# Performance work log

Measured on AMD Instinct MI355X. Metric: run time of the kernel, lower is better.

## Reference

```python
import jax, jax.numpy as jnp
import numpy as np

WS = 8          # cubic window side
HEADS = 6
DIM = 192


def _make_buffers(ws=WS):
    # relative_coords_table: [1, 2w-1, 2w-1, 2w-1, 3], signed log-spaced in [-1,1]*? (Swin V2)
    c = np.arange(-(ws - 1), ws, dtype=np.float32)
    g = np.stack(np.meshgrid(c, c, c, indexing='ij'), axis=-1)[None]  # [1,15,15,15,3]
    g = g / (ws - 1) * 8.0
    table = np.sign(g) * np.log2(np.abs(g) + 1.0) / np.log2(8.0)
    # relative_position_index: [N, N] into the (2w-1)^3 table
    coords = np.stack(np.meshgrid(np.arange(ws), np.arange(ws), np.arange(ws), indexing='ij'))
    cf = coords.reshape(3, -1)                          # [3, N]
    rel = cf[:, :, None] - cf[:, None, :]               # [3, N, N]
    rel = rel.transpose(1, 2, 0) + (ws - 1)             # [N, N, 3]
    idx = rel[..., 0] * (2 * ws - 1) ** 2 + rel[..., 1] * (2 * ws - 1) + rel[..., 2]
    return table.astype(np.float32), idx.astype(np.int32)


def setup_inputs() -> dict:
    key = jax.random.key(0)
    ks = jax.random.split(key, 8)
    B_, N, C, nW = 64, WS ** 3, DIM, 16
    table, idx = _make_buffers()
    return {
        'x': jax.random.normal(ks[0], (B_, N, C), jnp.float32),
        'mask': jax.random.normal(ks[1], (nW, N, N), jnp.float32),
        'qkv_w': jax.random.normal(ks[2], (3 * C, C), jnp.float32) * 0.05,
        'q_bias': jnp.zeros((C,), jnp.float32),
        'v_bias': jnp.zeros((C,), jnp.float32),
        'logit_scale': jnp.log(10.0) * jnp.ones((HEADS, 1, 1), jnp.float32),
        'cpb_w1': jax.random.normal(ks[3], (512, 3), jnp.float32) * 0.1,
        'cpb_b1': jnp.zeros((512,), jnp.float32),
        'cpb_w2': jax.random.normal(ks[4], (HEADS, 512), jnp.float32) * 0.1,
        'proj_w': jax.random.normal(ks[5], (C, C), jnp.float32) * 0.05,
        'proj_b': jnp.zeros((C,), jnp.float32),
        'rel_table': jnp.asarray(table),
        'rel_index': jnp.asarray(idx),
    }


def reference(x, mask, qkv_w, q_bias, v_bias, logit_scale, cpb_w1, cpb_b1,
              cpb_w2, proj_w, proj_b, rel_table, rel_index):
    B_, N, C = x.shape
    H = HEADS
    hd = C // H
    # qkv projection with (q_bias, 0, v_bias)
    qkv_b = jnp.concatenate([q_bias, jnp.zeros_like(v_bias), v_bias])
    qkv = (x @ qkv_w.T + qkv_b).reshape(B_, N, 3, H, hd).transpose(2, 0, 3, 1, 4)
    q, k, v = qkv[0], qkv[1], qkv[2]                 # each [B_, H, N, hd]
    # cosine attention with clamped learned logit scale
    qn = q / jnp.maximum(jnp.linalg.norm(q, axis=-1, keepdims=True), 1e-12)
    kn = k / jnp.maximum(jnp.linalg.norm(k, axis=-1, keepdims=True), 1e-12)
    scale = jnp.exp(jnp.minimum(logit_scale, jnp.log(100.0)))  # [H,1,1]
    attn = jnp.einsum('bhnd,bhmd->bhnm', qn, kn) * scale[None]
    # continuous position bias: MLP over coords table, gather by relative index
    hidden = jax.nn.relu(rel_table @ cpb_w1.T + cpb_b1)        # [1,15,15,15,512]
    tbl = (hidden @ cpb_w2.T).reshape(-1, H)                   # [3375, H]
    bias = tbl[rel_index.reshape(-1)].reshape(N, N, H).transpose(2, 0, 1)
    bias = 16.0 * jax.nn.sigmoid(bias)                         # [H, N, N]
    attn = attn + bias[None]
    # window mask
    nW = mask.shape[0]
    attn = attn.reshape(B_ // nW, nW, H, N, N) + mask[None, :, None]
    attn = jax.nn.softmax(attn.reshape(B_, H, N, N), axis=-1)
    out = jnp.einsum('bhnm,bhmd->bhnd', attn, v)
    out = out.transpose(0, 2, 1, 3).reshape(B_, N, C)
    return out @ proj_w.T + proj_b
```

## Files before the change

### kernel.cpp

```cpp
#include <hip/hip_runtime.h>
#include <hip/hip_bf16.h>
#include <math.h>

#define B__ 64
#define NTOK 512
#define CDIM 192
#define HEADS 6
#define HD 32
#define NW 16
#define T3 3375
#define HID 512

typedef _Float16 f16x8 __attribute__((ext_vector_type(8)));
typedef _Float16 f16x4 __attribute__((ext_vector_type(4)));
typedef float    f32x4 __attribute__((ext_vector_type(4)));

__global__ __launch_bounds__(512) void k_cpb(
    const float* __restrict__ rel_table, const float* __restrict__ w1,
    const float* __restrict__ b1, const float* __restrict__ w2,
    float* __restrict__ tbl_t) {
  int i = blockIdx.x;
  int t = threadIdx.x;
  float t0 = rel_table[i*3+0], t1 = rel_table[i*3+1], t2 = rel_table[i*3+2];
  float hval = fmaxf(t0*w1[t*3+0] + t1*w1[t*3+1] + t2*w1[t*3+2] + b1[t], 0.f);
  __shared__ float red[8][6];
  int wv = t >> 6, lane = t & 63;
  #pragma unroll
  for (int hh = 0; hh < 6; ++hh) {
    float p = hval * w2[hh*HID + t];
    #pragma unroll
    for (int off = 32; off > 0; off >>= 1) p += __shfl_down(p, off);
    if (lane == 0) red[wv][hh] = p;
  }
  __syncthreads();
  if (t < 6) {
    float s = 0.f;
    #pragma unroll
    for (int w8 = 0; w8 < 8; ++w8) s += red[w8][t];
    tbl_t[t*T3 + i] = 16.f / (1.f + __expf(-s));
  }
}

__global__ __launch_bounds__(64) void k_biasf(
    const int* __restrict__ idx, const float* __restrict__ tbl_t,
    _Float16* __restrict__ bias_f) {
  int bx = blockIdx.x;
  int h  = blockIdx.y;
  int l  = threadIdx.x;
  int qt = bx >> 5, kt = bx & 31;
  int k  = kt*16 + (l & 15);
  int qb = qt*16 + (l >> 4)*4;
  f16x4 v;
  #pragma unroll
  for (int r = 0; r < 4; ++r) {
    int id = idx[(qb + r)*512 + k];
    v[r] = (_Float16)tbl_t[h*T3 + id];
  }
  *(f16x4*)(bias_f + ((size_t)(h*1024 + bx)*64 + l)*4) = v;
}

__global__ __launch_bounds__(64) void k_maskf(
    const float* __restrict__ mask, _Float16* __restrict__ mask_f) {
  int bx = blockIdx.x;
  int w  = blockIdx.y;
  int l  = threadIdx.x;
  int qt = bx >> 5, kt = bx & 31;
  int k  = kt*16 + (l & 15);
  int qb = qt*16 + (l >> 4)*4;
  const float* mp = mask + (size_t)w*262144;
  f16x4 v;
  #pragma unroll
  for (int r = 0; r < 4; ++r)
    v[r] = (_Float16)mp[(qb + r)*512 + k];
  *(f16x4*)(mask_f + ((size_t)(w*1024 + bx)*64 + l)*4) = v;
}

__global__ __launch_bounds__(256) void k_xh(
    const float* __restrict__ x, _Float16* __restrict__ xh) {
  int i = blockIdx.x*256 + threadIdx.x;
  float4 v = ((const float4*)x)[i];
  f16x4 h = {(_Float16)v.x, (_Float16)v.y, (_Float16)v.z, (_Float16)v.w};
  *(f16x4*)(xh + (size_t)i*4) = h;
}

__global__ __launch_bounds__(256) void k_wh(
    const float* __restrict__ qkv_w, const float* __restrict__ proj_w,
    _Float16* __restrict__ wh) {
  int i = blockIdx.x*256 + threadIdx.x;
  float4 v = (i < 27648) ? ((const float4*)qkv_w)[i] : ((const float4*)proj_w)[i - 27648];
  f16x4 h = {(_Float16)v.x, (_Float16)v.y, (_Float16)v.z, (_Float16)v.w};
  *(f16x4*)(wh + (size_t)i*4) = h;
}

__global__ __launch_bounds__(256) void k_qkv(
    const _Float16* __restrict__ xh, const _Float16* __restrict__ wh,
    const float* __restrict__ q_bias, const float* __restrict__ v_bias,
    const float* __restrict__ logit_scale,
    _Float16* __restrict__ qn, _Float16* __restrict__ kn, _Float16* __restrict__ vv) {
  int wid = threadIdx.x >> 6, l = threadIdx.x & 63;
  int lr = l & 15, lg = l >> 4;
  int m0 = blockIdx.x*128 + wid*32;
  int cb = blockIdx.y;
  int c0 = cb*64;
  int p  = cb/3;
  int pc0 = (cb - p*3)*64;
  int h0 = pc0 >> 5;

  const f32x4 zero = {0.f,0.f,0.f,0.f};
  f32x4 acc[2][4];
  #pragma unroll
  for (int mt = 0; mt < 2; ++mt)
    #pragma unroll
    for (int nt = 0; nt < 4; ++nt) acc[mt][nt] = zero;

  const _Float16* wb = wh + (size_t)c0*192;
  for (int kc = 0; kc < 6; ++kc) {
    int ko = kc*32 + lg*8;
    f16x8 a0 = *(const f16x8*)(xh + (size_t)(m0 + lr)*192 + ko);
    f16x8 a1 = *(const f16x8*)(xh + (size_t)(m0 + 16 + lr)*192 + ko);
    #pragma unroll
    for (int nt = 0; nt < 4; ++nt) {
      f16x8 bf = *(const f16x8*)(wb + (size_t)(nt*16 + lr)*192 + ko);
      acc[0][nt] = __builtin_amdgcn_mfma_f32_16x16x32_f16(a0, bf, acc[0][nt], 0, 0, 0);
      acc[1][nt] = __builtin_amdgcn_mfma_f32_16x16x32_f16(a1, bf, acc[1][nt], 0, 0, 0);
    }
  }

  if (p == 0) {
    float bq[4];
    #pragma unroll
    for (int nt = 0; nt < 4; ++nt) bq[nt] = q_bias[pc0 + nt*16 + lr];
    float s0 = __expf(fminf(logit_scale[h0], 4.6051702f));
    float s1 = __expf(fminf(logit_scale[h0+1], 4.6051702f));
    #pragma unroll
    for (int mt = 0; mt < 2; ++mt) {
      #pragma unroll
      for (int nt = 0; nt < 4; ++nt)
        #pragma unroll
        for (int r = 0; r < 4; ++r) acc[mt][nt][r] += bq[nt];
      #pragma unroll
      for (int r = 0; r < 4; ++r) {
        float ss0 = acc[mt][0][r]*acc[mt][0][r] + acc[mt][1][r]*acc[mt][1][r];
        float ss1 = acc[mt][2][r]*acc[mt][2][r] + acc[mt][3][r]*acc[mt][3][r];
        #pragma unroll
        for (int off = 1; off < 16; off <<= 1) {
          ss0 += __shfl_xor(ss0, off);
          ss1 += __shfl_xor(ss1, off);
        }
        float inv0 = s0 / fmaxf(sqrtf(ss0), 1e-12f);
        float inv1 = s1 / fmaxf(sqrtf(ss1), 1e-12f);
        int m = m0 + mt*16 + lg*4 + r;
        int b = m >> 9, n = m & 511;
        #pragma unroll
        for (int nt = 0; nt < 4; ++nt) {
          int h = h0 + (nt >> 1);
          int d = (nt & 1)*16 + lr;
          float val = acc[mt][nt][r] * ((nt < 2) ? inv0 : inv1);
          qn[(((size_t)b*HEADS + h)*NTOK + n)*HD + d] = (_Float16)val;
        }
      }
    }
  } else if (p == 1) {
    #pragma unroll
    for (int mt = 0; mt < 2; ++mt) {
      #pragma unroll
      for (int r = 0; r < 4; ++r) {
        float ss0 = acc[mt][0][r]*acc[mt][0][r] + acc[mt][1][r]*acc[mt][1][r];
        float ss1 = acc[mt][2][r]*acc[mt][2][r] + acc[mt][3][r]*acc[mt][3][r];
        #pragma unroll
        for (int off = 1; off < 16; off <<= 1) {
          ss0 += __shfl_xor(ss0, off);
          ss1 += __shfl_xor(ss1, off);
        }
        float inv0 = 1.f / fmaxf(sqrtf(ss0), 1e-12f);
        float inv1 = 1.f / fmaxf(sqrtf(ss1), 1e-12f);
        int m = m0 + mt*16 + lg*4 + r;
        int b = m >> 9, n = m & 511;
        #pragma unroll
        for (int nt = 0; nt < 4; ++nt) {
          int h = h0 + (nt >> 1);
          int d = (nt & 1)*16 + lr;
          float val = acc[mt][nt][r] * ((nt < 2) ? inv0 : inv1);
          kn[(((size_t)b*HEADS + h)*NTOK + n)*HD + d] = (_Float16)val;
        }
      }
    }
  } else {
    float bv[4];
    #pragma unroll
    for (int nt = 0; nt < 4; ++nt) bv[nt] = v_bias[pc0 + nt*16 + lr];
    #pragma unroll
    for (int mt = 0; mt < 2; ++mt)
      #pragma unroll
      for (int r = 0; r < 4; ++r) {
        int m = m0 + mt*16 + lg*4 + r;
        int b = m >> 9, n = m & 511;
        #pragma unroll
        for (int nt = 0; nt < 4; ++nt) {
          int h = h0 + (nt >> 1);
          int d = (nt & 1)*16 + lr;
          vv[(((size_t)b*HEADS + h)*NTOK + n)*HD + d] = (_Float16)(acc[mt][nt][r] + bv[nt]);
        }
      }
  }
}

__global__ __launch_bounds__(256) void k_vt(
    const _Float16* __restrict__ vv, _Float16* __restrict__ vt) {
  __shared__ _Float16 lt[64][40];
  int nc = blockIdx.x;
  int pair = blockIdx.y;
  int t = threadIdx.x;
  {
    int r = t >> 2, d0 = (t & 3) * 8;
    f16x8 v = *(const f16x8*)(vv + ((size_t)pair*512 + nc*64 + r)*32 + d0);
    *(f16x8*)(&lt[r][d0]) = v;
  }
  __syncthreads();
  {
    int d = t >> 3, n0 = (t & 7) * 8;
    f16x8 v;
    #pragma unroll
    for (int j = 0; j < 8; ++j) v[j] = lt[n0 + j][d];
    *(f16x8*)(vt + ((size_t)pair*32 + d)*512 + nc*64 + n0) = v;
  }
}

__global__ __launch_bounds__(256) void k_attn(
    const _Float16* __restrict__ qn, const _Float16* __restrict__ kn,
    const _Float16* __restrict__ vt, const _Float16* __restrict__ bias_f,
    const _Float16* __restrict__ mask_f, _Float16* __restrict__ ao_h) {
  __shared__ _Float16 plds[4][32][88];
  int qblk = blockIdx.x, h = blockIdx.y, b = blockIdx.z;
  int w = b & (NW-1);
  int wid = threadIdx.x >> 6, l = threadIdx.x & 63;
  int lr = l & 15, lg = l >> 4;
  size_t pair = (size_t)b*HEADS + h;
  const _Float16* qb = qn + pair*NTOK*HD;
  const _Float16* kb = kn + pair*NTOK*HD;
  const _Float16* vb = vt + pair*HD*NTOK;
  const _Float16* bias_base = bias_f + (size_t)h*262144;
  const _Float16* mask_base = mask_f + (size_t)w*262144;
  int q0 = qblk*128 + wid*32;
  int qtb = q0 >> 4;

  f16x8 aq[2];
  aq[0] = *(const f16x8*)(qb + (size_t)(q0 + lr)*HD + lg*8);
  aq[1] = *(const f16x8*)(qb + (size_t)(q0 + 16 + lr)*HD + lg*8);

  const f32x4 zero = {0.f, 0.f, 0.f, 0.f};
  f32x4 o[2][2];
  o[0][0] = zero; o[0][1] = zero; o[1][0] = zero; o[1][1] = zero;
  float mrun[2][4], lrun[2][4];
  #pragma unroll
  for (int mt = 0; mt < 2; ++mt)
    #pragma unroll
    for (int r = 0; r < 4; ++r) { mrun[mt][r] = -1e30f; lrun[mt][r] = 0.f; }

  for (int ch = 0; ch < 8; ++ch) {
    f16x8 bk[4];
    #pragma unroll
    for (int nt = 0; nt < 4; ++nt)
      bk[nt] = *(const f16x8*)(kb + (size_t)(ch*64 + nt*16 + lr)*HD + lg*8);
    f32x4 s[2][4];
    #pragma unroll
    for (int mt = 0; mt < 2; ++mt)
      #pragma unroll
      for (int nt = 0; nt < 4; ++nt)
        s[mt][nt] = __builtin_amdgcn_mfma_f32_16x16x32_f16(aq[mt], bk[nt], zero, 0, 0, 0);
    #pragma unroll
    for (int mt = 0; mt < 2; ++mt) {
      int qt = qtb + mt;
      #pragma unroll
      for (int nt = 0; nt < 4; ++nt) {
        int kt = ch*4 + nt;
        size_t toff = ((size_t)(qt*32 + kt)*64 + l)*4;
        f16x4 bf = *(const f16x4*)(bias_base + toff);
        f16x4 mf = *(const f16x4*)(mask_base + toff);
        #pragma unroll
        for (int r = 0; r < 4; ++r)
          s[mt][nt][r] += (float)bf[r] + (float)mf[r];
      }
    }
    #pragma unroll
    for (int mt = 0; mt < 2; ++mt) {
      #pragma unroll
      for (int r = 0; r < 4; ++r) {
        float cm = fmaxf(fmaxf(s[mt][0][r], s[mt][1][r]), fmaxf(s[mt][2][r], s[mt][3][r]));
        cm = fmaxf(cm, __shfl_xor(cm, 1));
        cm = fmaxf(cm, __shfl_xor(cm, 2));
        cm = fmaxf(cm, __shfl_xor(cm, 4));
        cm = fmaxf(cm, __shfl_xor(cm, 8));
        float mold = mrun[mt][r];
        float mnew = fmaxf(mold, cm);
        float corr = __expf(mold - mnew);
        mrun[mt][r] = mnew;
        lrun[mt][r] *= corr;
        o[mt][0][r] *= corr;
        o[mt][1][r] *= corr;
        float rs = 0.f;
        #pragma unroll
        for (int nt = 0; nt < 4; ++nt) {
          float p = __expf(s[mt][nt][r] - mnew);
          s[mt][nt][r] = p;
          rs += p;
        }
        rs += __shfl_xor(rs, 1);
        rs += __shfl_xor(rs, 2);
        rs += __shfl_xor(rs, 4);
        rs += __shfl_xor(rs, 8);
        lrun[mt][r] += rs;
      }
    }
    #pragma unroll
    for (int mt = 0; mt < 2; ++mt)
      #pragma unroll
      for (int nt = 0; nt < 4; ++nt)
        #pragma unroll
        for (int r = 0; r < 4; ++r)
          plds[wid][mt*16 + lg*4 + r][nt*16 + lr] = (_Float16)s[mt][nt][r];
    #pragma unroll
    for (int kk = 0; kk < 2; ++kk) {
      f16x8 ap0 = *(const f16x8*)(&plds[wid][lr][kk*32 + lg*8]);
      f16x8 ap1 = *(const f16x8*)(&plds[wid][16 + lr][kk*32 + lg*8]);
      #pragma unroll
      for (int dt = 0; dt < 2; ++dt) {
        f16x8 bv = *(const f16x8*)(vb + (size_t)(dt*16 + lr)*NTOK + ch*64 + kk*32 + lg*8);
        o[0][dt] = __builtin_amdgcn_mfma_f32_16x16x32_f16(ap0, bv, o[0][dt], 0, 0, 0);
        o[1][dt] = __builtin_amdgcn_mfma_f32_16x16x32_f16(ap1, bv, o[1][dt], 0, 0, 0);
      }
    }
  }
  _Float16* op = ao_h + (size_t)b*NTOK*CDIM + (size_t)h*HD;
  #pragma unroll
  for (int mt = 0; mt < 2; ++mt) {
    #pragma unroll
    for (int r = 0; r < 4; ++r) {
      float inv = 1.f / lrun[mt][r];
      int qg = q0 + mt*16 + lg*4 + r;
      #pragma unroll
      for (int dt = 0; dt < 2; ++dt)
        op[(size_t)qg*CDIM + dt*16 + lr] = (_Float16)(o[mt][dt][r] * inv);
    }
  }
}

__global__ __launch_bounds__(256) void k_proj(
    const _Float16* __restrict__ ao_h, const _Float16* __restrict__ pw,
    const float* __restrict__ pb, float* __restrict__ out) {
  int wid = threadIdx.x >> 6, l = threadIdx.x & 63;
  int lr = l & 15, lg = l >> 4;
  int m0 = blockIdx.x*128 + wid*32;
  int c0 = blockIdx.y*64;

  const f32x4 zero = {0.f,0.f,0.f,0.f};
  f32x4 acc[2][4];
  #pragma unroll
  for (int mt = 0; mt < 2; ++mt)
    #pragma unroll
    for (int nt = 0; nt < 4; ++nt) acc[mt][nt] = zero;

  for (int kc = 0; kc < 6; ++kc) {
    int ko = kc*32 + lg*8;
    f16x8 a0 = *(const f16x8*)(ao_h + (size_t)(m0 + lr)*192 + ko);
    f16x8 a1 = *(const f16x8*)(ao_h + (size_t)(m0 + 16 + lr)*192 + ko);
    #pragma unroll
    for (int nt = 0; nt < 4; ++nt) {
      f16x8 bf = *(const f16x8*)(pw + (size_t)(c0 + nt*16 + lr)*192 + ko);
      acc[0][nt] = __builtin_amdgcn_mfma_f32_16x16x32_f16(a0, bf, acc[0][nt], 0, 0, 0);
      acc[1][nt] = __builtin_amdgcn_mfma_f32_16x16x32_f16(a1, bf, acc[1][nt], 0, 0, 0);
    }
  }

  float bias[4];
  #pragma unroll
  for (int nt = 0; nt < 4; ++nt) bias[nt] = pb[c0 + nt*16 + lr];
  #pragma unroll
  for (int mt = 0; mt < 2; ++mt)
    #pragma unroll
    for (int r = 0; r < 4; ++r) {
      int m = m0 + mt*16 + lg*4 + r;
      #pragma unroll
      for (int nt = 0; nt < 4; ++nt)
        out[(size_t)m*CDIM + c0 + nt*16 + lr] = acc[mt][nt][r] + bias[nt];
    }
}

extern "C" void kernel_launch(void* const* d_in, const int* in_sizes, int n_in,
                              void* d_out, int out_size, void* d_ws, size_t ws_size,
                              hipStream_t stream) {
  const float* x           = (const float*)d_in[0];
  const float* mask        = (const float*)d_in[1];
  const float* qkv_w       = (const float*)d_in[2];
  const float* q_bias      = (const float*)d_in[3];
  const float* v_bias      = (const float*)d_in[4];
  const float* logit_scale = (const float*)d_in[5];
  const float* cpb_w1      = (const float*)d_in[6];
  const float* cpb_b1      = (const float*)d_in[7];
  const float* cpb_w2      = (const float*)d_in[8];
  const float* proj_w      = (const float*)d_in[9];
  const float* proj_b      = (const float*)d_in[10];
  const float* rel_table   = (const float*)d_in[11];
  const int*   rel_index   = (const int*)d_in[12];
  float* out = (float*)d_out;

  float* wsf = (float*)d_ws;
  float* tbl_t = wsf;
  _Float16* hws    = (_Float16*)(wsf + 20480);
  _Float16* qn     = hws;
  _Float16* kn     = qn + 6291456;
  _Float16* vv     = kn + 6291456;
  _Float16* vt     = vv + 6291456;
  _Float16* bias_f = vt + 6291456;
  _Float16* mask_f = bias_f + 1572864;
  _Float16* xh     = mask_f + 4194304;
  _Float16* wh     = xh + 6291456;
  _Float16* ao_h   = wh + 147456;

  k_cpb<<<T3, 512, 0, stream>>>(rel_table, cpb_w1, cpb_b1, cpb_w2, tbl_t);
  k_biasf<<<dim3(1024, HEADS), 64, 0, stream>>>(rel_index, tbl_t, bias_f);
  k_maskf<<<dim3(1024, NW), 64, 0, stream>>>(mask, mask_f);
  k_xh<<<6144, 256, 0, stream>>>(x, xh);
  k_wh<<<144, 256, 0, stream>>>(qkv_w, proj_w, wh);
  k_qkv<<<dim3(256, 9), 256, 0, stream>>>(xh, wh, q_bias, v_bias, logit_scale, qn, kn, vv);
  k_vt<<<dim3(8, 384), 256, 0, stream>>>(vv, vt);
  k_attn<<<dim3(4, HEADS, B__), 256, 0, stream>>>(qn, kn, vt, bias_f, mask_f, ao_h);
  k_proj<<<dim3(256, 3), 256, 0, stream>>>(ao_h, wh + 110592, proj_b, out);
}
```

Baseline: 279.0 us.

## Fuse bias and mask into one precombined table, transpose S and use lazy rescaling

Bias and mask are merged into one fp16 table per (head, window), prescaled by log2e, and fed as the MFMA accumulator init so the QK^T result already includes them. The S tile is computed transposed so each lane owns one query row, which removes the per-row shuffle reductions. Softmax uses exp2 with a lazy rescale that only fires when the running max grows by more than a threshold. The V transpose kernel is removed because k_qkv writes V^T directly. The merged table is larger (96 slices instead of 22), adding memory traffic and workspace, and the lazy threshold lets unnormalised fp16 probabilities grow to about 2^8.

```diff
diff --git a/kernel.cpp b/kernel.cpp
--- a/kernel.cpp
+++ b/kernel.cpp
@@ -10,10 +10,17 @@
 #define NW 16
 #define T3 3375
 #define HID 512
+#define LOG2E 1.4426950408889634f
 
 typedef _Float16 f16x8 __attribute__((ext_vector_type(8)));
 typedef _Float16 f16x4 __attribute__((ext_vector_type(4)));
 typedef float    f32x4 __attribute__((ext_vector_type(4)));
+
+#if __has_builtin(__builtin_amdgcn_exp2f)
+#define EXP2F(x) __builtin_amdgcn_exp2f(x)
+#else
+#define EXP2F(x) __expf(0.69314718056f*(x))
+#endif
 
 __global__ __launch_bounds__(512) void k_cpb(
     const float* __restrict__ rel_table, const float* __restrict__ w1,
@@ -41,38 +48,24 @@
   }
 }
 
-__global__ __launch_bounds__(64) void k_biasf(
+__global__ __launch_bounds__(64) void k_bm(
     const int* __restrict__ idx, const float* __restrict__ tbl_t,
-    _Float16* __restrict__ bias_f) {
+    const float* __restrict__ mask, _Float16* __restrict__ bm) {
   int bx = blockIdx.x;
-  int h  = blockIdx.y;
-  int l  = threadIdx.x;
+  int hw = blockIdx.y;
+  int h = hw >> 4, w = hw & 15;
+  int l = threadIdx.x;
   int qt = bx >> 5, kt = bx & 31;
-  int k  = kt*16 + (l & 15);
-  int qb = qt*16 + (l >> 4)*4;
+  int q  = qt*16 + (l & 15);
+  int k0 = kt*16 + (l >> 4)*4;
+  const float* mp = mask + (size_t)w*262144 + (size_t)q*512 + k0;
+  const int*   ip = idx + (size_t)q*512 + k0;
+  const float* tb = tbl_t + (size_t)h*T3;
   f16x4 v;
   #pragma unroll
-  for (int r = 0; r < 4; ++r) {
-    int id = idx[(qb + r)*512 + k];
-    v[r] = (_Float16)tbl_t[h*T3 + id];
-  }
-  *(f16x4*)(bias_f + ((size_t)(h*1024 + bx)*64 + l)*4) = v;
-}
-
-__global__ __launch_bounds__(64) void k_maskf(
-    const float* __restrict__ mask, _Float16* __restrict__ mask_f) {
-  int bx = blockIdx.x;
-  int w  = blockIdx.y;
-  int l  = threadIdx.x;
-  int qt = bx >> 5, kt = bx & 31;
-  int k  = kt*16 + (l & 15);
-  int qb = qt*16 + (l >> 4)*4;
-  const float* mp = mask + (size_t)w*262144;
-  f16x4 v;
-  #pragma unroll
   for (int r = 0; r < 4; ++r)
-    v[r] = (_Float16)mp[(qb + r)*512 + k];
-  *(f16x4*)(mask_f + ((size_t)(w*1024 + bx)*64 + l)*4) = v;
+    v[r] = (_Float16)(LOG2E * (tb[ip[r]] + mp[r]));
+  *(f16x4*)(bm + ((size_t)hw*1024 + bx)*256 + l*4) = v;
 }
 
 __global__ __launch_bounds__(256) void k_xh(
@@ -96,7 +89,7 @@
     const _Float16* __restrict__ xh, const _Float16* __restrict__ wh,
     const float* __restrict__ q_bias, const float* __restrict__ v_bias,
     const float* __restrict__ logit_scale,
-    _Float16* __restrict__ qn, _Float16* __restrict__ kn, _Float16* __restrict__ vv) {
+    _Float16* __restrict__ qn, _Float16* __restrict__ kn, _Float16* __restrict__ vt) {
   int wid = threadIdx.x >> 6, l = threadIdx.x & 63;
   int lr = l & 15, lg = l >> 4;
   int m0 = blockIdx.x*128 + wid*32;
@@ -130,8 +123,8 @@
     float bq[4];
     #pragma unroll
     for (int nt = 0; nt < 4; ++nt) bq[nt] = q_bias[pc0 + nt*16 + lr];
-    float s0 = __expf(fminf(logit_scale[h0], 4.6051702f));
-    float s1 = __expf(fminf(logit_scale[h0+1], 4.6051702f));
+    float s0 = __expf(fminf(logit_scale[h0], 4.6051702f)) * LOG2E;
+    float s1 = __expf(fminf(logit_scale[h0+1], 4.6051702f)) * LOG2E;
     #pragma unroll
     for (int mt = 0; mt < 2; ++mt) {
       #pragma unroll
@@ -190,46 +183,26 @@
     #pragma unroll
     for (int nt = 0; nt < 4; ++nt) bv[nt] = v_bias[pc0 + nt*16 + lr];
     #pragma unroll
-    for (int mt = 0; mt < 2; ++mt)
-      #pragma unroll
-      for (int r = 0; r < 4; ++r) {
-        int m = m0 + mt*16 + lg*4 + r;
-        int b = m >> 9, n = m & 511;
-        #pragma unroll
-        for (int nt = 0; nt < 4; ++nt) {
-          int h = h0 + (nt >> 1);
-          int d = (nt & 1)*16 + lr;
-          vv[(((size_t)b*HEADS + h)*NTOK + n)*HD + d] = (_Float16)(acc[mt][nt][r] + bv[nt]);
-        }
-      }
-  }
-}
-
-__global__ __launch_bounds__(256) void k_vt(
-    const _Float16* __restrict__ vv, _Float16* __restrict__ vt) {
-  __shared__ _Float16 lt[64][40];
-  int nc = blockIdx.x;
-  int pair = blockIdx.y;
-  int t = threadIdx.x;
-  {
-    int r = t >> 2, d0 = (t & 3) * 8;
-    f16x8 v = *(const f16x8*)(vv + ((size_t)pair*512 + nc*64 + r)*32 + d0);
-    *(f16x8*)(&lt[r][d0]) = v;
-  }
-  __syncthreads();
-  {
-    int d = t >> 3, n0 = (t & 7) * 8;
-    f16x8 v;
-    #pragma unroll
-    for (int j = 0; j < 8; ++j) v[j] = lt[n0 + j][d];
-    *(f16x8*)(vt + ((size_t)pair*32 + d)*512 + nc*64 + n0) = v;
+    for (int mt = 0; mt < 2; ++mt) {
+      int m = m0 + mt*16 + lg*4;
+      int b = m >> 9, n = m & 511;
+      #pragma unroll
+      for (int nt = 0; nt < 4; ++nt) {
+        int h = h0 + (nt >> 1);
+        int d = (nt & 1)*16 + lr;
+        f16x4 hv;
+        #pragma unroll
+        for (int r = 0; r < 4; ++r) hv[r] = (_Float16)(acc[mt][nt][r] + bv[nt]);
+        *(f16x4*)(vt + (((size_t)b*HEADS + h)*HD + d)*NTOK + n) = hv;
+      }
+    }
   }
 }
 
 __global__ __launch_bounds__(256) void k_attn(
     const _Float16* __restrict__ qn, const _Float16* __restrict__ kn,
-    const _Float16* __restrict__ vt, const _Float16* __restrict__ bias_f,
-    const _Float16* __restrict__ mask_f, _Float16* __restrict__ ao_h) {
+    const _Float16* __restrict__ vt, const _Float16* __restrict__ bm,
+    _Float16* __restrict__ ao_h) {
   __shared__ _Float16 plds[4][32][88];
   int qblk = blockIdx.x, h = blockIdx.y, b = blockIdx.z;
   int w = b & (NW-1);
@@ -239,8 +212,7 @@
   const _Float16* qb = qn + pair*NTOK*HD;
   const _Float16* kb = kn + pair*NTOK*HD;
   const _Float16* vb = vt + pair*HD*NTOK;
-  const _Float16* bias_base = bias_f + (size_t)h*262144;
-  const _Float16* mask_base = mask_f + (size_t)w*262144;
+  const _Float16* bm_base = bm + ((size_t)(h*16 + w)*1024)*256;
   int q0 = qblk*128 + wid*32;
   int qtb = q0 >> 4;
 
@@ -251,74 +223,63 @@
   const f32x4 zero = {0.f, 0.f, 0.f, 0.f};
   f32x4 o[2][2];
   o[0][0] = zero; o[0][1] = zero; o[1][0] = zero; o[1][1] = zero;
-  float mrun[2][4], lrun[2][4];
-  #pragma unroll
-  for (int mt = 0; mt < 2; ++mt)
-    #pragma unroll
-    for (int r = 0; r < 4; ++r) { mrun[mt][r] = -1e30f; lrun[mt][r] = 0.f; }
+  float mrun[2] = {-1e30f, -1e30f};
+  float lrun[2] = {0.f, 0.f};
 
   for (int ch = 0; ch < 8; ++ch) {
     f16x8 bk[4];
     #pragma unroll
-    for (int nt = 0; nt < 4; ++nt)
-      bk[nt] = *(const f16x8*)(kb + (size_t)(ch*64 + nt*16 + lr)*HD + lg*8);
+    for (int kt = 0; kt < 4; ++kt)
+      bk[kt] = *(const f16x8*)(kb + (size_t)(ch*64 + kt*16 + lr)*HD + lg*8);
     f32x4 s[2][4];
     #pragma unroll
-    for (int mt = 0; mt < 2; ++mt)
-      #pragma unroll
-      for (int nt = 0; nt < 4; ++nt)
-        s[mt][nt] = __builtin_amdgcn_mfma_f32_16x16x32_f16(aq[mt], bk[nt], zero, 0, 0, 0);
-    #pragma unroll
-    for (int mt = 0; mt < 2; ++mt) {
-      int qt = qtb + mt;
-      #pragma unroll
-      for (int nt = 0; nt < 4; ++nt) {
-        int kt = ch*4 + nt;
-        size_t toff = ((size_t)(qt*32 + kt)*64 + l)*4;
-        f16x4 bf = *(const f16x4*)(bias_base + toff);
-        f16x4 mf = *(const f16x4*)(mask_base + toff);
-        #pragma unroll
-        for (int r = 0; r < 4; ++r)
-          s[mt][nt][r] += (float)bf[r] + (float)mf[r];
-      }
-    }
-    #pragma unroll
-    for (int mt = 0; mt < 2; ++mt) {
-      #pragma unroll
-      for (int r = 0; r < 4; ++r) {
-        float cm = fmaxf(fmaxf(s[mt][0][r], s[mt][1][r]), fmaxf(s[mt][2][r], s[mt][3][r]));
-        cm = fmaxf(cm, __shfl_xor(cm, 1));
-        cm = fmaxf(cm, __shfl_xor(cm, 2));
-        cm = fmaxf(cm, __shfl_xor(cm, 4));
-        cm = fmaxf(cm, __shfl_xor(cm, 8));
-        float mold = mrun[mt][r];
-        float mnew = fmaxf(mold, cm);
-        float corr = __expf(mold - mnew);
-        mrun[mt][r] = mnew;
-        lrun[mt][r] *= corr;
-        o[mt][0][r] *= corr;
-        o[mt][1][r] *= corr;
-        float rs = 0.f;
-        #pragma unroll
-        for (int nt = 0; nt < 4; ++nt) {
-          float p = __expf(s[mt][nt][r] - mnew);
-          s[mt][nt][r] = p;
+    for (int mt = 0; mt < 2; ++mt) {
+      #pragma unroll
+      for (int kt = 0; kt < 4; ++kt) {
+        size_t toff = ((size_t)((qtb + mt)*32 + ch*4 + kt))*256 + l*4;
+        f16x4 c4 = *(const f16x4*)(bm_base + toff);
+        f32x4 cf = {(float)c4[0], (float)c4[1], (float)c4[2], (float)c4[3]};
+        s[mt][kt] = __builtin_amdgcn_mfma_f32_16x16x32_f16(bk[kt], aq[mt], cf, 0, 0, 0);
+      }
+    }
+    #pragma unroll
+    for (int mt = 0; mt < 2; ++mt) {
+      float pm = s[mt][0][0];
+      #pragma unroll
+      for (int kt = 0; kt < 4; ++kt)
+        #pragma unroll
+        for (int r = 0; r < 4; ++r) pm = fmaxf(pm, s[mt][kt][r]);
+      pm = fmaxf(pm, __shfl_xor(pm, 16));
+      pm = fmaxf(pm, __shfl_xor(pm, 32));
+      if (!__all(pm <= mrun[mt] + 8.f)) {
+        float mnew = fmaxf(mrun[mt], pm);
+        float corr = EXP2F(mrun[mt] - mnew);
+        lrun[mt] *= corr;
+        mrun[mt] = mnew;
+        #pragma unroll
+        for (int r = 0; r < 4; ++r) {
+          float cr = __shfl(corr, (l >> 4)*4 + r);
+          o[mt][0][r] *= cr;
+          o[mt][1][r] *= cr;
+        }
+      }
+      float mref = mrun[mt];
+      float rs = 0.f;
+      #pragma unroll
+      for (int kt = 0; kt < 4; ++kt) {
+        f16x4 pv;
+        #pragma unroll
+        for (int r = 0; r < 4; ++r) {
+          float p = EXP2F(s[mt][kt][r] - mref);
+          pv[r] = (_Float16)p;
           rs += p;
         }
-        rs += __shfl_xor(rs, 1);
-        rs += __shfl_xor(rs, 2);
-        rs += __shfl_xor(rs, 4);
-        rs += __shfl_xor(rs, 8);
-        lrun[mt][r] += rs;
-      }
-    }
-    #pragma unroll
-    for (int mt = 0; mt < 2; ++mt)
-      #pragma unroll
-      for (int nt = 0; nt < 4; ++nt)
-        #pragma unroll
-        for (int r = 0; r < 4; ++r)
-          plds[wid][mt*16 + lg*4 + r][nt*16 + lr] = (_Float16)s[mt][nt][r];
+        *(f16x4*)(&plds[wid][mt*16 + lr][kt*16 + lg*4]) = pv;
+      }
+      rs += __shfl_xor(rs, 16);
+      rs += __shfl_xor(rs, 32);
+      lrun[mt] += rs;
+    }
     #pragma unroll
     for (int kk = 0; kk < 2; ++kk) {
       f16x8 ap0 = *(const f16x8*)(&plds[wid][lr][kk*32 + lg*8]);
@@ -334,13 +295,14 @@
   _Float16* op = ao_h + (size_t)b*NTOK*CDIM + (size_t)h*HD;
   #pragma unroll
   for (int mt = 0; mt < 2; ++mt) {
+    float inv = 1.f / lrun[mt];
     #pragma unroll
     for (int r = 0; r < 4; ++r) {
-      float inv = 1.f / lrun[mt][r];
+      float iv = __shfl(inv, (l >> 4)*4 + r);
       int qg = q0 + mt*16 + lg*4 + r;
       #pragma unroll
       for (int dt = 0; dt < 2; ++dt)
-        op[(size_t)qg*CDIM + dt*16 + lr] = (_Float16)(o[mt][dt][r] * inv);
+        op[(size_t)qg*CDIM + dt*16 + lr] = (_Float16)(o[mt][dt][r] * iv);
     }
   }
 }
@@ -406,24 +368,20 @@
 
   float* wsf = (float*)d_ws;
   float* tbl_t = wsf;
-  _Float16* hws    = (_Float16*)(wsf + 20480);
-  _Float16* qn     = hws;
-  _Float16* kn     = qn + 6291456;
-  _Float16* vv     = kn + 6291456;
-  _Float16* vt     = vv + 6291456;
-  _Float16* bias_f = vt + 6291456;
-  _Float16* mask_f = bias_f + 1572864;
-  _Float16* xh     = mask_f + 4194304;
-  _Float16* wh     = xh + 6291456;
-  _Float16* ao_h   = wh + 147456;
+  _Float16* hws = (_Float16*)(wsf + 20480);
+  _Float16* qn  = hws;
+  _Float16* kn  = qn + 6291456;
+  _Float16* vt  = kn + 6291456;
+  _Float16* bm  = vt + 6291456;
+  _Float16* wh  = bm + 25165824;
+  _Float16* xh  = wh + 147456;
+  _Float16* ao_h = xh;
 
   k_cpb<<<T3, 512, 0, stream>>>(rel_table, cpb_w1, cpb_b1, cpb_w2, tbl_t);
-  k_biasf<<<dim3(1024, HEADS), 64, 0, stream>>>(rel_index, tbl_t, bias_f);
-  k_maskf<<<dim3(1024, NW), 64, 0, stream>>>(mask, mask_f);
+  k_bm<<<dim3(1024, 96), 64, 0, stream>>>(rel_index, tbl_t, mask, bm);
   k_xh<<<6144, 256, 0, stream>>>(x, xh);
   k_wh<<<144, 256, 0, stream>>>(qkv_w, proj_w, wh);
-  k_qkv<<<dim3(256, 9), 256, 0, stream>>>(xh, wh, q_bias, v_bias, logit_scale, qn, kn, vv);
-  k_vt<<<dim3(8, 384), 256, 0, stream>>>(vv, vt);
-  k_attn<<<dim3(4, HEADS, B__), 256, 0, stream>>>(qn, kn, vt, bias_f, mask_f, ao_h);
+  k_qkv<<<dim3(256, 9), 256, 0, stream>>>(xh, wh, q_bias, v_bias, logit_scale, qn, kn, vt);
+  k_attn<<<dim3(4, HEADS, B__), 256, 0, stream>>>(qn, kn, vt, bm, ao_h);
   k_proj<<<dim3(256, 3), 256, 0, stream>>>(ao_h, wh + 110592, proj_b, out);
 }
```

New measurement: 295.0 us. 5.7% more time.
